# Kernel optimization log

Measured on AMD Instinct MI355X. Metric: run time of the kernel, lower is better.

Reference implementation:

```python
import jax, jax.numpy as jnp
import numpy as np

EMBED_DIM = 1024
NUM_HEADS = 16
HEAD_DIM = EMBED_DIM // NUM_HEADS


def setup_inputs() -> dict:
    key = jax.random.key(0)
    k1, k2, k3, k4, k5 = jax.random.split(key, 5)
    B, S, D = 2, 2048, EMBED_DIM
    s_in = 1.0 / np.sqrt(D)
    x = jax.random.normal(k1, (B, S, D), dtype=jnp.float32)
    W_qkv = jax.random.uniform(k2, (D, 3 * D), dtype=jnp.float32, minval=-s_in, maxval=s_in)
    b_qkv = jax.random.uniform(k3, (3 * D,), dtype=jnp.float32, minval=-s_in, maxval=s_in)
    W_out = jax.random.uniform(k4, (D, D), dtype=jnp.float32, minval=-s_in, maxval=s_in)
    b_out = jax.random.uniform(k5, (D,), dtype=jnp.float32, minval=-s_in, maxval=s_in)
    return {"x": x, "W_qkv": W_qkv, "b_qkv": b_qkv, "W_out": W_out, "b_out": b_out}


def reference(x, W_qkv, b_qkv, W_out, b_out):
    B, S, D = x.shape
    H, Hd = NUM_HEADS, HEAD_DIM
    qkv = x @ W_qkv + b_qkv                      # [B,S,3D]
    qkv = qkv.reshape(B, S, 3, H, Hd)
    q = qkv[:, :, 0].transpose(0, 2, 1, 3)       # [B,H,S,Hd]
    k = qkv[:, :, 1].transpose(0, 2, 1, 3)
    v = qkv[:, :, 2].transpose(0, 2, 1, 3)
    scores = jnp.einsum('bhsd,bhtd->bhst', q, k) / jnp.sqrt(jnp.float32(Hd))
    attn = jax.nn.softmax(scores, axis=-1)       # dropout is identity in eval mode
    out = jnp.einsum('bhst,bhtd->bhsd', attn, v)
    out = out.transpose(0, 2, 1, 3).reshape(B, S, D)
    return out @ W_out + b_out
```

## Files before the change

### kernel.cpp

```cpp
#include <hip/hip_runtime.h>
#include <stdint.h>
#include <math.h>

#define EMBED 1024
#define HEADS 16
#define HDIM  64
#define SEQ   2048
#define BATCH 2

typedef __bf16 bf16x8 __attribute__((ext_vector_type(8)));
typedef float  f32x4  __attribute__((ext_vector_type(4)));
typedef unsigned short u16x8 __attribute__((ext_vector_type(8)));
typedef unsigned short u16x4 __attribute__((ext_vector_type(4)));
typedef uint32_t u32x4v __attribute__((ext_vector_type(4)));

static __device__ __forceinline__ unsigned short f2bf(float f){
  union { float f; uint32_t u; } v; v.f = f;
  uint32_t u = v.u;
  uint32_t r = (u + 0x7FFFu + ((u >> 16) & 1u)) >> 16;
  return (unsigned short)r;
}
static __device__ __forceinline__ bf16x8 as_bf(u16x8 v){ return __builtin_bit_cast(bf16x8, v); }

static __device__ __forceinline__ uint32_t pk_bf16(float a, float b){
#if defined(__has_builtin) && __has_builtin(__builtin_amdgcn_cvt_pk_bf16_f32)
  typedef __bf16 bf16x2 __attribute__((ext_vector_type(2)));
  bf16x2 p = __builtin_amdgcn_cvt_pk_bf16_f32(a, b);
  return __builtin_bit_cast(uint32_t, p);
#else
  return (uint32_t)f2bf(a) | ((uint32_t)f2bf(b) << 16);
#endif
}

static __device__ __forceinline__ float fexp2(float x){
#if defined(__has_builtin) && __has_builtin(__builtin_amdgcn_exp2f)
  return __builtin_amdgcn_exp2f(x);
#else
  return exp2f(x);
#endif
}

static __device__ __forceinline__ void stage16(const unsigned short* gp,
                                               unsigned short* lp_wave, int lane){
#if defined(__has_builtin) && __has_builtin(__builtin_amdgcn_global_load_lds)
  __builtin_amdgcn_global_load_lds((const __attribute__((address_space(1))) void*)gp,
                                   (__attribute__((address_space(3))) void*)lp_wave,
                                   16, 0, 0);
#else
  *(u16x8*)(lp_wave + lane * 8) = *(const u16x8*)gp;
#endif
}

__global__ __launch_bounds__(256) void prep(
    const float* __restrict__ x,      unsigned short* __restrict__ xb,
    const float* __restrict__ W_qkv,  unsigned short* __restrict__ wqkvT)
{
  __shared__ unsigned short T[32 * 36];
  const int bid = blockIdx.x;
  const int t   = threadIdx.x;

  if (bid < 4096){
    int i = (bid * 256 + t) * 4;
    float4 v = *(const float4*)(x + i);
    u16x4 o;
    o[0] = f2bf(v.x); o[1] = f2bf(v.y); o[2] = f2bf(v.z); o[3] = f2bf(v.w);
    *(u16x4*)(xb + i) = o;
    return;
  }
  int idx = bid - 4096;
  int n0 = (idx % 96) * 32, k0 = (idx / 96) * 32;
  int kr = t >> 3, nc = (t & 7) * 4;
  float4 wv = *(const float4*)(W_qkv + (size_t)(k0 + kr) * 3072 + n0 + nc);
  T[(nc + 0) * 36 + kr] = f2bf(wv.x);
  T[(nc + 1) * 36 + kr] = f2bf(wv.y);
  T[(nc + 2) * 36 + kr] = f2bf(wv.z);
  T[(nc + 3) * 36 + kr] = f2bf(wv.w);
  __syncthreads();
  int nr = t >> 3, kc = (t & 7) * 4;
  *(u16x4*)(wqkvT + (size_t)(n0 + nr) * 1024 + k0 + kc) = *(const u16x4*)&T[nr * 36 + kc];
}

__global__ __launch_bounds__(256) void wtrans_out(const float* __restrict__ W,
                                                  unsigned short* __restrict__ Wt){
  __shared__ unsigned short T[32 * 36];
  int t = threadIdx.x;
  int n0 = blockIdx.x * 32, k0 = blockIdx.y * 32;
  int kr = t >> 3, nc = (t & 7) * 4;
  float4 wv = *(const float4*)(W + (size_t)(k0 + kr) * 1024 + n0 + nc);
  T[(nc + 0) * 36 + kr] = f2bf(wv.x);
  T[(nc + 1) * 36 + kr] = f2bf(wv.y);
  T[(nc + 2) * 36 + kr] = f2bf(wv.z);
  T[(nc + 3) * 36 + kr] = f2bf(wv.w);
  __syncthreads();
  int nr = t >> 3, kc = (t & 7) * 4;
  *(u16x4*)(Wt + (size_t)(n0 + nr) * 1024 + k0 + kc) = *(const u16x4*)&T[nr * 36 + kc];
}

__global__ __launch_bounds__(256) void vtrans(const unsigned short* __restrict__ V,
                                              unsigned short* __restrict__ VT){
  __shared__ unsigned short T[32 * 36];
  int t = threadIdx.x;
  int s0 = blockIdx.x * 32, d0 = blockIdx.y * 32;
  size_t base = (size_t)blockIdx.z * SEQ * HDIM;
  int sr = t >> 3, dc = (t & 7) * 4;
  u16x4 vv = *(const u16x4*)(V + base + (size_t)(s0 + sr) * HDIM + d0 + dc);
  T[(dc + 0) * 36 + sr] = vv[0];
  T[(dc + 1) * 36 + sr] = vv[1];
  T[(dc + 2) * 36 + sr] = vv[2];
  T[(dc + 3) * 36 + sr] = vv[3];
  __syncthreads();
  int dr = t >> 3, sc = (t & 7) * 4;
  int pos = (((sc >> 2) & 3) << 3) + (((sc >> 4) & 1) << 2);
  *(u16x4*)(VT + base + (size_t)(d0 + dr) * SEQ + s0 + pos) = *(const u16x4*)&T[dr * 36 + sc];
}

__global__ __launch_bounds__(256) void gemm_qkv(
    const unsigned short* __restrict__ A,
    const unsigned short* __restrict__ Bt,
    const float* __restrict__ bias,
    unsigned short* __restrict__ q_ws,
    unsigned short* __restrict__ k_ws,
    unsigned short* __restrict__ v_ws,
    int M, int N, int K)
{
  __shared__ unsigned short As[128 * 32];
  __shared__ unsigned short Bs[128 * 32];
  const int tid  = threadIdx.x;
  const int bm   = blockIdx.y, bn = blockIdx.x;
  const int w    = tid >> 6, lane = tid & 63;
  const int quad = lane >> 4, l16 = lane & 15;
  const int wm   = (w >> 1) * 64, wn = (w & 1) * 64;

  f32x4 acc[4][4] = {};

  for (int k0 = 0; k0 < K; k0 += 32) {
    #pragma unroll
    for (int i = 0; i < 2; i++){
      int c = w + i * 4;
      int row = c * 16 + (lane >> 2);
      int kg = (lane & 3) ^ (row & 3);
      stage16(A  + (size_t)(bm * 128 + row) * K + k0 + kg * 8, &As[c * 512], lane);
      stage16(Bt + (size_t)(bn * 128 + row) * K + k0 + kg * 8, &Bs[c * 512], lane);
    }
    __syncthreads();

    bf16x8 af[4], bfr[4];
    #pragma unroll
    for (int t = 0; t < 4; t++){
      int ra = wm + t * 16 + l16;
      int rb = wn + t * 16 + l16;
      af[t]  = as_bf(*(const u16x8*)&As[(ra << 5) + ((quad ^ (ra & 3)) << 3)]);
      bfr[t] = as_bf(*(const u16x8*)&Bs[(rb << 5) + ((quad ^ (rb & 3)) << 3)]);
    }
    #pragma unroll
    for (int mt = 0; mt < 4; mt++)
      #pragma unroll
      for (int nt = 0; nt < 4; nt++)
        acc[mt][nt] = __builtin_amdgcn_mfma_f32_16x16x32_bf16(af[mt], bfr[nt], acc[mt][nt], 0, 0, 0);
    __syncthreads();
  }

  const int which = (bn * 128) >> 10;
  unsigned short* dst = (which == 0) ? q_ws : (which == 1) ? k_ws : v_ws;
  const float scale = (which == 0) ? 0.18033688f : 1.0f;
  const int b = bm >> 4;
  #pragma unroll
  for (int nt = 0; nt < 4; nt++){
    int gnb = bn * 128 + wn + nt * 16;
    int h   = (gnb & 1023) >> 6;
    int hd  = (gnb & 63) + l16;
    float bv = bias[gnb + l16];
    unsigned short* dp = dst + (size_t)(b * HEADS + h) * SEQ * HDIM + hd;
    #pragma unroll
    for (int mt = 0; mt < 4; mt++){
      int s0 = ((bm & 15) * 128) + wm + mt * 16 + quad * 4;
      #pragma unroll
      for (int r = 0; r < 4; r++)
        dp[(size_t)(s0 + r) * HDIM] = f2bf((acc[mt][nt][r] + bv) * scale);
    }
  }
}

__global__ __launch_bounds__(256) void gemm_out(
    const unsigned short* __restrict__ A,
    const unsigned short* __restrict__ Bt,
    const float* __restrict__ bias,
    float* __restrict__ Cout,
    int M, int N, int K)
{
  __shared__ unsigned short As[128 * 32];
  __shared__ unsigned short Bs[64 * 32];
  const int tid  = threadIdx.x;
  const int bm   = blockIdx.y, bn = blockIdx.x;
  const int w    = tid >> 6, lane = tid & 63;
  const int quad = lane >> 4, l16 = lane & 15;
  const int wm   = (w >> 1) * 64, wn = (w & 1) * 32;

  f32x4 acc[4][2] = {};

  for (int k0 = 0; k0 < K; k0 += 32) {
    #pragma unroll
    for (int i = 0; i < 2; i++){
      int c = w + i * 4;
      int row = c * 16 + (lane >> 2);
      int kg = (lane & 3) ^ (row & 3);
      stage16(A + (size_t)(bm * 128 + row) * K + k0 + kg * 8, &As[c * 512], lane);
    }
    {
      int c = w;
      int row = c * 16 + (lane >> 2);
      int kg = (lane & 3) ^ (row & 3);
      stage16(Bt + (size_t)(bn * 64 + row) * K + k0 + kg * 8, &Bs[c * 512], lane);
    }
    __syncthreads();

    bf16x8 af[4], bfr[2];
    #pragma unroll
    for (int t = 0; t < 4; t++){
      int ra = wm + t * 16 + l16;
      af[t] = as_bf(*(const u16x8*)&As[(ra << 5) + ((quad ^ (ra & 3)) << 3)]);
    }
    #pragma unroll
    for (int t = 0; t < 2; t++){
      int rb = wn + t * 16 + l16;
      bfr[t] = as_bf(*(const u16x8*)&Bs[(rb << 5) + ((quad ^ (rb & 3)) << 3)]);
    }
    #pragma unroll
    for (int mt = 0; mt < 4; mt++)
      #pragma unroll
      for (int nt = 0; nt < 2; nt++)
        acc[mt][nt] = __builtin_amdgcn_mfma_f32_16x16x32_bf16(af[mt], bfr[nt], acc[mt][nt], 0, 0, 0);
    __syncthreads();
  }

  #pragma unroll
  for (int mt = 0; mt < 4; mt++)
    #pragma unroll
    for (int nt = 0; nt < 2; nt++)
      #pragma unroll
      for (int r = 0; r < 4; r++){
        int gm = bm * 128 + wm + mt * 16 + quad * 4 + r;
        int gn = bn * 64 + wn + nt * 16 + l16;
        Cout[(size_t)gm * N + gn] = acc[mt][nt][r] + bias[gn];
      }
}

__global__ __launch_bounds__(512) void attn(
    const unsigned short* __restrict__ q_ws,
    const unsigned short* __restrict__ k_ws,
    const unsigned short* __restrict__ vt_ws,
    unsigned short* __restrict__ o_ws)
{
  __shared__ unsigned short Qs[128 * 64];
  __shared__ unsigned short Ks[2][64 * 64];
  __shared__ unsigned short VTs[2][64 * 64];
  const int tid  = threadIdx.x;
  const int qt   = blockIdx.x, bh = blockIdx.y;
  const int w    = tid >> 6, lane = tid & 63;
  const int quad = lane >> 4, l16 = lane & 15;
  const size_t base = (size_t)bh * SEQ * HDIM;

  #pragma unroll
  for (int i = 0; i < 2; i++){
    int c = w * 2 + i;
    int row = c * 8 + (lane >> 3);
    int kg = (lane & 7) ^ (row & 7);
    stage16(q_ws + base + (size_t)(qt * 128 + row) * HDIM + kg * 8, &Qs[c * 512], lane);
  }

  const int srow = w * 8 + (lane >> 3);
  const int skg  = (lane & 7) ^ (srow & 7);
  const int dofs = w * 512 + lane * 8;

  stage16(k_ws  + base + (size_t)srow * HDIM + skg * 8, &Ks[0][w * 512],  lane);
  stage16(vt_ws + base + (size_t)srow * SEQ + skg * 8,  &VTs[0][w * 512], lane);
  __syncthreads();

  bf16x8 bq[2];
  {
    int row = w * 16 + l16;
    #pragma unroll
    for (int ks = 0; ks < 2; ks++)
      bq[ks] = as_bf(*(const u16x8*)&Qs[(row << 6) + ((((ks << 2) + quad) ^ (row & 7)) << 3)]);
  }

  const unsigned short* kp = k_ws  + base + (size_t)(64 + srow) * HDIM + skg * 8;
  const unsigned short* vp = vt_ws + base + (size_t)srow * SEQ + 64 + skg * 8;

  f32x4 acc[4] = {};
  float li = 0.f;

  for (int kt = 0; kt < SEQ / 64; kt++){
    const int cur = kt & 1;
    u16x8 kpre, vpre;
    if (kt < SEQ / 64 - 1){
      kpre = *(const u16x8*)kp;  kp += 64 * HDIM;
      vpre = *(const u16x8*)vp;  vp += 64;
    }

    f32x4 sf[4] = {};
    #pragma unroll
    for (int ks = 0; ks < 2; ks++){
      #pragma unroll
      for (int nt = 0; nt < 4; nt++){
        int rk = nt * 16 + l16;
        bf16x8 ak = as_bf(*(const u16x8*)&Ks[cur][(rk << 6) + ((((ks << 2) + quad) ^ (rk & 7)) << 3)]);
        sf[nt] = __builtin_amdgcn_mfma_f32_16x16x32_bf16(ak, bq[ks], sf[nt], 0, 0, 0);
      }
    }

    #pragma unroll
    for (int nt = 0; nt < 4; nt++)
      #pragma unroll
      for (int r = 0; r < 4; r++)
        sf[nt][r] = fexp2(sf[nt][r]);
    #pragma unroll
    for (int nt = 0; nt < 4; nt++)
      li += (sf[nt][0] + sf[nt][1]) + (sf[nt][2] + sf[nt][3]);

    #pragma unroll
    for (int c = 0; c < 2; c++){
      u32x4v aw;
      aw[0] = pk_bf16(sf[c * 2][0],     sf[c * 2][1]);
      aw[1] = pk_bf16(sf[c * 2][2],     sf[c * 2][3]);
      aw[2] = pk_bf16(sf[c * 2 + 1][0], sf[c * 2 + 1][1]);
      aw[3] = pk_bf16(sf[c * 2 + 1][2], sf[c * 2 + 1][3]);
      bf16x8 ap = __builtin_bit_cast(bf16x8, aw);
      #pragma unroll
      for (int nt = 0; nt < 4; nt++){
        int rv = nt * 16 + l16;
        bf16x8 bv = as_bf(*(const u16x8*)&VTs[cur][(rv << 6) + ((((c << 2) + quad) ^ (rv & 7)) << 3)]);
        acc[nt] = __builtin_amdgcn_mfma_f32_16x16x32_bf16(ap, bv, acc[nt], 0, 0, 0);
      }
    }

    if (kt < SEQ / 64 - 1){
      *(u16x8*)&Ks[cur ^ 1][dofs]  = kpre;
      *(u16x8*)&VTs[cur ^ 1][dofs] = vpre;
    }
    __syncthreads();
  }

  li += __shfl_xor(li, 16);
  li += __shfl_xor(li, 32);
  float inv = 1.0f / li;
  float invr[4];
  #pragma unroll
  for (int r = 0; r < 4; r++)
    invr[r] = __shfl(inv, quad * 4 + r);

  int b = bh >> 4, h = bh & 15;
  #pragma unroll
  for (int nt = 0; nt < 4; nt++)
    #pragma unroll
    for (int r = 0; r < 4; r++){
      int s = qt * 128 + w * 16 + quad * 4 + r;
      int d = h * 64 + nt * 16 + l16;
      o_ws[((size_t)(b * SEQ + s)) * EMBED + d] = f2bf(acc[nt][r] * invr[r]);
    }
}

extern "C" void kernel_launch(void* const* d_in, const int* in_sizes, int n_in,
                              void* d_out, int out_size, void* d_ws, size_t ws_size,
                              hipStream_t stream) {
  const float* x     = (const float*)d_in[0];
  const float* W_qkv = (const float*)d_in[1];
  const float* b_qkv = (const float*)d_in[2];
  const float* W_out = (const float*)d_in[3];
  const float* b_out = (const float*)d_in[4];
  float* out = (float*)d_out;

  char* ws = (char*)d_ws;
  unsigned short* xb    = (unsigned short*)(ws);
  unsigned short* q     = (unsigned short*)(ws + ((size_t)8  << 20));
  unsigned short* k     = (unsigned short*)(ws + ((size_t)16 << 20));
  unsigned short* v     = (unsigned short*)(ws + ((size_t)24 << 20));
  unsigned short* woutT = (unsigned short*)(ws + ((size_t)24 << 20));
  unsigned short* vt    = (unsigned short*)(ws + ((size_t)32 << 20));
  unsigned short* wqkvT = (unsigned short*)(ws + ((size_t)32 << 20));
  unsigned short* o     = xb;

  prep<<<dim3(7168), dim3(256), 0, stream>>>(x, xb, W_qkv, wqkvT);

  gemm_qkv<<<dim3(24, 32), dim3(256), 0, stream>>>(
      xb, wqkvT, b_qkv, q, k, v, 4096, 3072, 1024);

  vtrans<<<dim3(64, 2, 32), dim3(256), 0, stream>>>(v, vt);

  wtrans_out<<<dim3(32, 32), dim3(256), 0, stream>>>(W_out, woutT);

  attn<<<dim3(16, 32), dim3(512), 0, stream>>>(q, k, vt, o);

  gemm_out<<<dim3(16, 32), dim3(256), 0, stream>>>(
      o, woutT, b_out, out, 4096, 1024, 1024);
}
```

Before: 198.0 us.

## Double query rows per attention block to reuse K/V tiles across two query subtiles

Each attention block now processes 256 query rows instead of 128, with each wave holding two 16-row query fragments and reusing every K and V^T LDS fragment for both. The goal is to halve K/V global and LDS traffic per query and raise MFMA density per LDS read. The key loop is unrolled by two so the double-buffer index is compile-time. In exchange the grid drops to 256 blocks, which may underfill the 256 CUs, and register pressure roughly doubles for accumulators and scores.

Result: no change. 197.8 us (-0.1%).

```diff
diff --git a/kernel.cpp b/kernel.cpp
--- a/kernel.cpp
+++ b/kernel.cpp
@@ -251,7 +251,7 @@
     const unsigned short* __restrict__ vt_ws,
     unsigned short* __restrict__ o_ws)
 {
-  __shared__ unsigned short Qs[128 * 64];
+  __shared__ unsigned short Qs[256 * 64];
   __shared__ unsigned short Ks[2][64 * 64];
   __shared__ unsigned short VTs[2][64 * 64];
   const int tid  = threadIdx.x;
@@ -261,11 +261,11 @@
   const size_t base = (size_t)bh * SEQ * HDIM;
 
   #pragma unroll
-  for (int i = 0; i < 2; i++){
-    int c = w * 2 + i;
+  for (int i = 0; i < 4; i++){
+    int c = w * 4 + i;
     int row = c * 8 + (lane >> 3);
     int kg = (lane & 7) ^ (row & 7);
-    stage16(q_ws + base + (size_t)(qt * 128 + row) * HDIM + kg * 8, &Qs[c * 512], lane);
+    stage16(q_ws + base + (size_t)(qt * 256 + row) * HDIM + kg * 8, &Qs[c * 512], lane);
   }
 
   const int srow = w * 8 + (lane >> 3);
@@ -276,88 +276,112 @@
   stage16(vt_ws + base + (size_t)srow * SEQ + skg * 8,  &VTs[0][w * 512], lane);
   __syncthreads();
 
-  bf16x8 bq[2];
-  {
-    int row = w * 16 + l16;
+  bf16x8 bq[2][2];
+  #pragma unroll
+  for (int mq = 0; mq < 2; mq++){
+    int row = w * 32 + mq * 16 + l16;
     #pragma unroll
     for (int ks = 0; ks < 2; ks++)
-      bq[ks] = as_bf(*(const u16x8*)&Qs[(row << 6) + ((((ks << 2) + quad) ^ (row & 7)) << 3)]);
+      bq[mq][ks] = as_bf(*(const u16x8*)&Qs[(row << 6) + ((((ks << 2) + quad) ^ (row & 7)) << 3)]);
   }
 
   const unsigned short* kp = k_ws  + base + (size_t)(64 + srow) * HDIM + skg * 8;
   const unsigned short* vp = vt_ws + base + (size_t)srow * SEQ + 64 + skg * 8;
 
-  f32x4 acc[4] = {};
-  float li = 0.f;
-
-  for (int kt = 0; kt < SEQ / 64; kt++){
-    const int cur = kt & 1;
-    u16x8 kpre, vpre;
-    if (kt < SEQ / 64 - 1){
-      kpre = *(const u16x8*)kp;  kp += 64 * HDIM;
-      vpre = *(const u16x8*)vp;  vp += 64;
-    }
-
-    f32x4 sf[4] = {};
-    #pragma unroll
-    for (int ks = 0; ks < 2; ks++){
-      #pragma unroll
-      for (int nt = 0; nt < 4; nt++){
-        int rk = nt * 16 + l16;
-        bf16x8 ak = as_bf(*(const u16x8*)&Ks[cur][(rk << 6) + ((((ks << 2) + quad) ^ (rk & 7)) << 3)]);
-        sf[nt] = __builtin_amdgcn_mfma_f32_16x16x32_bf16(ak, bq[ks], sf[nt], 0, 0, 0);
-      }
-    }
-
+  f32x4 acc[2][4] = {};
+  float li[2] = {0.f, 0.f};
+
+  for (int kt2 = 0; kt2 < SEQ / 128; kt2++){
+    #pragma unroll
+    for (int half = 0; half < 2; half++){
+      const int cur = half;
+      const int kt  = kt2 * 2 + half;
+      u16x8 kpre, vpre;
+      if (kt < SEQ / 64 - 1){
+        kpre = *(const u16x8*)kp;  kp += 64 * HDIM;
+        vpre = *(const u16x8*)vp;  vp += 64;
+      }
+
+      f32x4 sf[4][2] = {};
+      #pragma unroll
+      for (int ks = 0; ks < 2; ks++){
+        #pragma unroll
+        for (int nt = 0; nt < 4; nt++){
+          int rk = nt * 16 + l16;
+          bf16x8 ak = as_bf(*(const u16x8*)&Ks[cur][(rk << 6) + ((((ks << 2) + quad) ^ (rk & 7)) << 3)]);
+          #pragma unroll
+          for (int mq = 0; mq < 2; mq++)
+            sf[nt][mq] = __builtin_amdgcn_mfma_f32_16x16x32_bf16(ak, bq[mq][ks], sf[nt][mq], 0, 0, 0);
+        }
+      }
+
+      #pragma unroll
+      for (int nt = 0; nt < 4; nt++)
+        #pragma unroll
+        for (int mq = 0; mq < 2; mq++)
+          #pragma unroll
+          for (int r = 0; r < 4; r++)
+            sf[nt][mq][r] = fexp2(sf[nt][mq][r]);
+      #pragma unroll
+      for (int mq = 0; mq < 2; mq++)
+        #pragma unroll
+        for (int nt = 0; nt < 4; nt++)
+          li[mq] += (sf[nt][mq][0] + sf[nt][mq][1]) + (sf[nt][mq][2] + sf[nt][mq][3]);
+
+      #pragma unroll
+      for (int c = 0; c < 2; c++){
+        bf16x8 ap[2];
+        #pragma unroll
+        for (int mq = 0; mq < 2; mq++){
+          u32x4v aw;
+          aw[0] = pk_bf16(sf[c * 2][mq][0],     sf[c * 2][mq][1]);
+          aw[1] = pk_bf16(sf[c * 2][mq][2],     sf[c * 2][mq][3]);
+          aw[2] = pk_bf16(sf[c * 2 + 1][mq][0], sf[c * 2 + 1][mq][1]);
+          aw[3] = pk_bf16(sf[c * 2 + 1][mq][2], sf[c * 2 + 1][mq][3]);
+          ap[mq] = __builtin_bit_cast(bf16x8, aw);
+        }
+        #pragma unroll
+        for (int nt = 0; nt < 4; nt++){
+          int rv = nt * 16 + l16;
+          bf16x8 bv = as_bf(*(const u16x8*)&VTs[cur][(rv << 6) + ((((c << 2) + quad) ^ (rv & 7)) << 3)]);
+          #pragma unroll
+          for (int mq = 0; mq < 2; mq++)
+            acc[mq][nt] = __builtin_amdgcn_mfma_f32_16x16x32_bf16(ap[mq], bv, acc[mq][nt], 0, 0, 0);
+        }
+      }
+
+      if (kt < SEQ / 64 - 1){
+        *(u16x8*)&Ks[cur ^ 1][dofs]  = kpre;
+        *(u16x8*)&VTs[cur ^ 1][dofs] = vpre;
+      }
+      __syncthreads();
+    }
+  }
+
+  #pragma unroll
+  for (int mq = 0; mq < 2; mq++){
+    li[mq] += __shfl_xor(li[mq], 16);
+    li[mq] += __shfl_xor(li[mq], 32);
+  }
+  float inv[2] = {1.0f / li[0], 1.0f / li[1]};
+  float invr[2][4];
+  #pragma unroll
+  for (int mq = 0; mq < 2; mq++)
+    #pragma unroll
+    for (int r = 0; r < 4; r++)
+      invr[mq][r] = __shfl(inv[mq], quad * 4 + r);
+
+  int b = bh >> 4, h = bh & 15;
+  #pragma unroll
+  for (int mq = 0; mq < 2; mq++)
     #pragma unroll
     for (int nt = 0; nt < 4; nt++)
       #pragma unroll
-      for (int r = 0; r < 4; r++)
-        sf[nt][r] = fexp2(sf[nt][r]);
-    #pragma unroll
-    for (int nt = 0; nt < 4; nt++)
-      li += (sf[nt][0] + sf[nt][1]) + (sf[nt][2] + sf[nt][3]);
-
-    #pragma unroll
-    for (int c = 0; c < 2; c++){
-      u32x4v aw;
-      aw[0] = pk_bf16(sf[c * 2][0],     sf[c * 2][1]);
-      aw[1] = pk_bf16(sf[c * 2][2],     sf[c * 2][3]);
-      aw[2] = pk_bf16(sf[c * 2 + 1][0], sf[c * 2 + 1][1]);
-      aw[3] = pk_bf16(sf[c * 2 + 1][2], sf[c * 2 + 1][3]);
-      bf16x8 ap = __builtin_bit_cast(bf16x8, aw);
-      #pragma unroll
-      for (int nt = 0; nt < 4; nt++){
-        int rv = nt * 16 + l16;
-        bf16x8 bv = as_bf(*(const u16x8*)&VTs[cur][(rv << 6) + ((((c << 2) + quad) ^ (rv & 7)) << 3)]);
-        acc[nt] = __builtin_amdgcn_mfma_f32_16x16x32_bf16(ap, bv, acc[nt], 0, 0, 0);
-      }
-    }
-
-    if (kt < SEQ / 64 - 1){
-      *(u16x8*)&Ks[cur ^ 1][dofs]  = kpre;
-      *(u16x8*)&VTs[cur ^ 1][dofs] = vpre;
-    }
-    __syncthreads();
-  }
-
-  li += __shfl_xor(li, 16);
-  li += __shfl_xor(li, 32);
-  float inv = 1.0f / li;
-  float invr[4];
-  #pragma unroll
-  for (int r = 0; r < 4; r++)
-    invr[r] = __shfl(inv, quad * 4 + r);
-
-  int b = bh >> 4, h = bh & 15;
-  #pragma unroll
-  for (int nt = 0; nt < 4; nt++)
-    #pragma unroll
-    for (int r = 0; r < 4; r++){
-      int s = qt * 128 + w * 16 + quad * 4 + r;
-      int d = h * 64 + nt * 16 + l16;
-      o_ws[((size_t)(b * SEQ + s)) * EMBED + d] = f2bf(acc[nt][r] * invr[r]);
-    }
+      for (int r = 0; r < 4; r++){
+        int s = qt * 256 + w * 32 + mq * 16 + quad * 4 + r;
+        int d = h * 64 + nt * 16 + l16;
+        o_ws[((size_t)(b * SEQ + s)) * EMBED + d] = f2bf(acc[mq][nt][r] * invr[mq][r]);
+      }
 }
 
 extern "C" void kernel_launch(void* const* d_in, const int* in_sizes, int n_in,
@@ -389,7 +413,7 @@
 
   wtrans_out<<<dim3(32, 32), dim3(256), 0, stream>>>(W_out, woutT);
 
-  attn<<<dim3(16, 32), dim3(512), 0, stream>>>(q, k, vt, o);
+  attn<<<dim3(8, 32), dim3(512), 0, stream>>>(q, k, vt, o);
 
   gemm_out<<<dim3(16, 32), dim3(256), 0, stream>>>(
       o, woutT, b_out, out, 4096, 1024, 1024);
```
